# Kernel optimization log

Hardware: AMD Instinct MI355X
Metric: run time of the kernel (lower is better)

## Reference

```python
import jax, jax.numpy as jnp
import numpy as np

N_EMBD = 2048
N_HEAD = 16
HEAD_DIM = N_EMBD // N_HEAD
MAX_SEQ = 2048
ROPE_BASE = 10000.0


def _build_rope_cache(seq_len, head_dim, base):
    theta = 1.0 / (base ** (jnp.arange(0, head_dim, 2, dtype=jnp.float32) / head_dim))
    idx_theta = jnp.arange(seq_len, dtype=jnp.float32)[:, None] * theta[None, :]  # [T, hd/2]
    return jnp.cos(idx_theta), jnp.sin(idx_theta)


def _apply_rope(x, cos, sin):
    # x: [B, T, H, hd]; interleaved (even, odd) pairing along last dim
    B, T, H, hd = x.shape
    xf = x.astype(jnp.float32).reshape(B, T, H, hd // 2, 2)
    x0, x1 = xf[..., 0], xf[..., 1]
    c = cos[None, :T, None, :]
    s = sin[None, :T, None, :]
    out = jnp.stack([x0 * c - x1 * s, x1 * c + x0 * s], axis=-1)
    return out.reshape(B, T, H, hd).astype(x.dtype)


def setup_inputs() -> dict:
    key = jax.random.key(0)
    k1, k2, k3 = jax.random.split(key, 3)
    x = jax.random.normal(k1, (2, 2048, N_EMBD), dtype=jnp.float32)
    # torch Linear(D, 3D, bias=False): y = x @ W.T ; store as [D, 3D] for x @ W
    scale = 1.0 / np.sqrt(N_EMBD)
    w_attn = jax.random.normal(k2, (N_EMBD, 3 * N_EMBD), dtype=jnp.float32) * scale
    w_proj = jax.random.normal(k3, (N_EMBD, N_EMBD), dtype=jnp.float32) * scale
    return {"x": x, "w_attn": w_attn, "w_proj": w_proj}


def reference(x, w_attn, w_proj):
    B, T, D = x.shape
    cos, sin = _build_rope_cache(MAX_SEQ, HEAD_DIM, ROPE_BASE)
    qkv = x @ w_attn                                   # [B, T, 3D]
    q, k, v = jnp.split(qkv, 3, axis=-1)
    q = q.reshape(B, T, N_HEAD, HEAD_DIM)
    k = k.reshape(B, T, N_HEAD, HEAD_DIM)
    v = v.reshape(B, T, N_HEAD, HEAD_DIM)
    q = _apply_rope(q, cos, sin)
    k = _apply_rope(k, cos, sin)
    # non-causal SDPA (original calls F.sdpa without is_causal)
    scale = 1.0 / jnp.sqrt(jnp.asarray(HEAD_DIM, dtype=q.dtype))
    scores = jnp.einsum("bqhd,bkhd->bhqk", q, k) * scale
    attn = jax.nn.softmax(scores, axis=-1)
    y = jnp.einsum("bhqk,bkhd->bqhd", attn, v).reshape(B, T, D)
    return y @ w_proj
```

## Files before the change

### kernel.cpp

```cpp
#include <hip/hip_runtime.h>
#include <cstdint>
#include <cstddef>

typedef __attribute__((ext_vector_type(8))) short bf16x8;
typedef __attribute__((ext_vector_type(8))) unsigned short us8;
typedef __attribute__((ext_vector_type(4))) float f32x4;

#define TSEQ 2048

__device__ __forceinline__ unsigned short f2bf(float f) {
  union { float f; uint32_t u; } v; v.f = f;
  uint32_t u = v.u;
  uint32_t r = (u + 0x7FFFu + ((u >> 16) & 1u)) >> 16;
  return (unsigned short)r;
}
__device__ __forceinline__ unsigned short f2bf_trunc(float f) {
  union { float f; uint32_t u; } v; v.f = f;
  return (unsigned short)(v.u >> 16);
}
__device__ __forceinline__ float bf2f(unsigned short h) {
  union { uint32_t u; float f; } v; v.u = ((uint32_t)h) << 16;
  return v.f;
}

__device__ __forceinline__ void async16(const void* g, void* l) {
  __builtin_amdgcn_global_load_lds(
      (const __attribute__((address_space(1))) unsigned int*)g,
      (__attribute__((address_space(3))) unsigned int*)l,
      16, 0, 0);
}

__global__ __launch_bounds__(256) void cvt_x(
    const float* __restrict__ in, unsigned short* __restrict__ out)
{
  const size_t i = ((size_t)blockIdx.x * 256 + threadIdx.x) * 16;
  f32x4 a0 = *(const f32x4*)(in + i);
  f32x4 a1 = *(const f32x4*)(in + i + 4);
  f32x4 a2 = *(const f32x4*)(in + i + 8);
  f32x4 a3 = *(const f32x4*)(in + i + 12);
  us8 lo, hi;
#pragma unroll
  for (int j = 0; j < 4; j++) {
    lo[j] = f2bf(a0[j]); lo[j + 4] = f2bf(a1[j]);
    hi[j] = f2bf(a2[j]); hi[j + 4] = f2bf(a3[j]);
  }
  *(us8*)(out + i) = lo;
  *(us8*)(out + i + 8) = hi;
}

__global__ __launch_bounds__(256) void transpose_w(
    const float* __restrict__ in, unsigned short* __restrict__ out,
    int R, int C)
{
  __shared__ unsigned short tile[32][33];
  const int bx = blockIdx.x * 32;
  const int by = blockIdx.y * 32;
  const int tx = threadIdx.x & 31;
  const int ty = threadIdx.x >> 5;
#pragma unroll
  for (int r = ty; r < 32; r += 8)
    tile[r][tx] = f2bf(in[(size_t)(by + r) * C + bx + tx]);
  __syncthreads();
#pragma unroll
  for (int r = ty; r < 32; r += 8)
    out[(size_t)(bx + r) * R + by + tx] = tile[tx][r];
}

template <int CF32>
__global__ __launch_bounds__(256) void gemm_bt(
    const unsigned short* __restrict__ A,
    const unsigned short* __restrict__ Bt,
    void* __restrict__ Cv,
    int M, int N, int K, int ldc)
{
  __shared__ unsigned short As[2][128 * 32];
  __shared__ unsigned short Bs[2][128 * 32];
  const int tid  = threadIdx.x;
  const int lane = tid & 63;
  const int w    = tid >> 6;
  const int m0   = blockIdx.y * 128;
  const int n0   = blockIdx.x * 128;
  const int wm   = (w & 1) * 64;
  const int wn   = (w >> 1) * 64;

  const int srow = lane >> 2;
  const int scol = (lane & 3) * 8;
  const unsigned short* ga0 = A  + (size_t)(m0 + w * 16 + srow) * K + scol;
  const unsigned short* ga1 = ga0 + (size_t)64 * K;
  const unsigned short* gb0 = Bt + (size_t)(n0 + w * 16 + srow) * K + scol;
  const unsigned short* gb1 = gb0 + (size_t)64 * K;

  f32x4 acc[4][4];
#pragma unroll
  for (int i = 0; i < 4; i++)
#pragma unroll
    for (int j = 0; j < 4; j++) acc[i][j] = (f32x4){0.f, 0.f, 0.f, 0.f};

  const int frow = lane & 15;
  const int fcol = (lane >> 4) * 8;

  for (int kt = 0; kt < K; kt += 64) {
    __syncthreads();
    async16(ga0 + kt,      &As[0][w * 512]);
    async16(ga1 + kt,      &As[0][(4 + w) * 512]);
    async16(ga0 + kt + 32, &As[1][w * 512]);
    async16(ga1 + kt + 32, &As[1][(4 + w) * 512]);
    async16(gb0 + kt,      &Bs[0][w * 512]);
    async16(gb1 + kt,      &Bs[0][(4 + w) * 512]);
    async16(gb0 + kt + 32, &Bs[1][w * 512]);
    async16(gb1 + kt + 32, &Bs[1][(4 + w) * 512]);
    __syncthreads();

#pragma unroll
    for (int h = 0; h < 2; h++) {
      bf16x8 af[4], bfr[4];
#pragma unroll
      for (int i = 0; i < 4; i++)
        af[i] = *(const bf16x8*)&As[h][(wm + i * 16 + frow) * 32 + fcol];
#pragma unroll
      for (int i = 0; i < 4; i++)
        bfr[i] = *(const bf16x8*)&Bs[h][(wn + i * 16 + frow) * 32 + fcol];
#pragma unroll
      for (int mi = 0; mi < 4; mi++)
#pragma unroll
        for (int ni = 0; ni < 4; ni++)
          acc[mi][ni] = __builtin_amdgcn_mfma_f32_16x16x32_bf16(
              af[mi], bfr[ni], acc[mi][ni], 0, 0, 0);
    }
  }

  const int crow0 = m0 + wm + (lane >> 4) * 4;
  const int ccol0 = n0 + wn + (lane & 15);
  if (CF32) {
    float* Cf = (float*)Cv;
#pragma unroll
    for (int mi = 0; mi < 4; mi++)
#pragma unroll
      for (int i = 0; i < 4; i++) {
        const int row = crow0 + mi * 16 + i;
#pragma unroll
        for (int ni = 0; ni < 4; ni++)
          Cf[(size_t)row * ldc + ccol0 + ni * 16] = acc[mi][ni][i];
      }
  } else {
    unsigned short* Cb = (unsigned short*)Cv;
#pragma unroll
    for (int mi = 0; mi < 4; mi++)
#pragma unroll
      for (int i = 0; i < 4; i++) {
        const int row = crow0 + mi * 16 + i;
#pragma unroll
        for (int ni = 0; ni < 4; ni++)
          Cb[(size_t)row * ldc + ccol0 + ni * 16] = f2bf(acc[mi][ni][i]);
      }
  }
}

__global__ __launch_bounds__(256) void rope_qk(unsigned short* __restrict__ qkv)
{
  const int p   = blockIdx.x * 256 + threadIdx.x;
  const int row = p >> 11;
  const int col = (p & 2047) * 2;
  const int t   = row & (TSEQ - 1);
  const int hd  = col & 127;
  const float theta = powf(10000.0f, -(float)hd * (1.0f / 128.0f));
  const float ang   = (float)t * theta;
  float s, c;
  sincosf(ang, &s, &c);
  const float sc = (col < 2048) ? 0.08838834764831845f : 1.0f;
  uint32_t* ptr = (uint32_t*)(qkv + (size_t)row * 6144 + col);
  const uint32_t u = *ptr;
  const float x0 = bf2f((unsigned short)(u & 0xffffu));
  const float x1 = bf2f((unsigned short)(u >> 16));
  const float o0 = (x0 * c - x1 * s) * sc;
  const float o1 = (x1 * c + x0 * s) * sc;
  *ptr = (uint32_t)f2bf(o0) | ((uint32_t)f2bf(o1) << 16);
}

__global__ __launch_bounds__(256) void repack_v(
    const unsigned short* __restrict__ qkv, unsigned short* __restrict__ Vtg)
{
  __shared__ unsigned short tile[32][33];
  const int tt = blockIdx.x * 32;
  const int dd = blockIdx.y * 32;
  const int bh = blockIdx.z;
  const int b  = bh >> 4, h = bh & 15;
  const int tx = threadIdx.x & 31;
  const int ty = threadIdx.x >> 5;
#pragma unroll
  for (int r = ty; r < 32; r += 8)
    tile[r][tx] = qkv[(size_t)(b * TSEQ + tt + r) * 6144 + 4096 + h * 128 + dd + tx];
  __syncthreads();
#pragma unroll
  for (int r = ty; r < 32; r += 8)
    Vtg[(size_t)bh * 262144 + (size_t)(dd + r) * TSEQ + tt + tx] = tile[tx][r];
}

__global__ __launch_bounds__(256) void attn(
    const unsigned short* __restrict__ qkv,
    const unsigned short* __restrict__ Vtg,
    unsigned short* __restrict__ y)
{
  __shared__ unsigned short Ks[64 * 136];
  __shared__ unsigned short Vs[144 * 72];
  __shared__ unsigned short Ps[4][32 * 72];

  const int tid  = threadIdx.x;
  const int lane = tid & 63;
  const int w    = tid >> 6;
  const int q0   = blockIdx.x * 128;
  const int h    = blockIdx.y;
  const int b    = blockIdx.z;
  const int bh   = b * 16 + h;
  const int quad = lane >> 4;
  const int l15  = lane & 15;
  const int kq   = quad * 8;

  for (int idx = tid; idx < 16 * 72; idx += 256)
    Vs[128 * 72 + idx] = (idx < 72) ? (unsigned short)0x3F80 : (unsigned short)0;

  bf16x8 qa[2][4];
#pragma unroll
  for (int mt = 0; mt < 2; mt++) {
    const unsigned short* gQ =
        qkv + (size_t)(b * TSEQ + q0 + w * 32 + mt * 16 + l15) * 6144 + h * 128 + kq;
#pragma unroll
    for (int dc = 0; dc < 4; dc++) qa[mt][dc] = *(const bf16x8*)(gQ + dc * 32);
  }

  f32x4 ot[2][9];
#pragma unroll
  for (int mt = 0; mt < 2; mt++)
#pragma unroll
    for (int nt = 0; nt < 9; nt++) ot[mt][nt] = (f32x4){0.f, 0.f, 0.f, 0.f};

  const int krow = tid >> 2;
  const int kd   = (tid & 3) * 32;
  const unsigned short* gK = qkv + (size_t)(b * TSEQ) * 6144 + 2048 + h * 128 + kd;
  const int vd = tid >> 1;
  const int vc = (tid & 1) * 32;
  const unsigned short* gVt = Vtg + (size_t)bh * 262144 + (size_t)vd * TSEQ + vc;

  for (int kb = 0; kb < TSEQ; kb += 64) {
    __syncthreads();
    {
      const unsigned short* pk = gK + (size_t)(kb + krow) * 6144;
#pragma unroll
      for (int j = 0; j < 4; j++)
        *(us8*)&Ks[krow * 136 + kd + j * 8] = *(const us8*)(pk + j * 8);
      const unsigned short* pv = gVt + kb;
#pragma unroll
      for (int j = 0; j < 4; j++)
        *(us8*)&Vs[vd * 72 + vc + j * 8] = *(const us8*)(pv + j * 8);
    }
    __syncthreads();

    f32x4 s[2][4];
#pragma unroll
    for (int mt = 0; mt < 2; mt++)
#pragma unroll
      for (int ct = 0; ct < 4; ct++) s[mt][ct] = (f32x4){0.f, 0.f, 0.f, 0.f};
#pragma unroll
    for (int dc = 0; dc < 4; dc++) {
#pragma unroll
      for (int ct = 0; ct < 4; ct++) {
        bf16x8 kf = *(const bf16x8*)&Ks[(ct * 16 + l15) * 136 + dc * 32 + kq];
        s[0][ct] = __builtin_amdgcn_mfma_f32_16x16x32_bf16(qa[0][dc], kf, s[0][ct], 0, 0, 0);
        s[1][ct] = __builtin_amdgcn_mfma_f32_16x16x32_bf16(qa[1][dc], kf, s[1][ct], 0, 0, 0);
      }
    }

    unsigned short* pw = &Ps[w][0];
#pragma unroll
    for (int mt = 0; mt < 2; mt++)
#pragma unroll
      for (int ct = 0; ct < 4; ct++)
#pragma unroll
        for (int i = 0; i < 4; i++)
          pw[(mt * 16 + quad * 4 + i) * 72 + ct * 16 + l15] =
              f2bf_trunc(__expf(fminf(s[mt][ct][i], 30.f)));

    __asm__ volatile("s_waitcnt lgkmcnt(0)" ::: "memory");

#pragma unroll
    for (int kc = 0; kc < 2; kc++) {
      bf16x8 pa0 = *(const bf16x8*)&pw[(l15) * 72 + kc * 32 + kq];
      bf16x8 pa1 = *(const bf16x8*)&pw[(16 + l15) * 72 + kc * 32 + kq];
#pragma unroll
      for (int nt = 0; nt < 9; nt++) {
        bf16x8 vb = *(const bf16x8*)&Vs[(nt * 16 + l15) * 72 + kc * 32 + kq];
        ot[0][nt] = __builtin_amdgcn_mfma_f32_16x16x32_bf16(pa0, vb, ot[0][nt], 0, 0, 0);
        ot[1][nt] = __builtin_amdgcn_mfma_f32_16x16x32_bf16(pa1, vb, ot[1][nt], 0, 0, 0);
      }
    }
  }

#pragma unroll
  for (int mt = 0; mt < 2; mt++) {
    unsigned short* gy =
        y + (size_t)(b * TSEQ + q0 + w * 32 + mt * 16 + quad * 4) * 2048 + h * 128 + l15;
#pragma unroll
    for (int i = 0; i < 4; i++) {
      const float inv = 1.0f / __shfl(ot[mt][8][i], lane & 48);
#pragma unroll
      for (int nt = 0; nt < 8; nt++)
        gy[(size_t)i * 2048 + nt * 16] = f2bf(ot[mt][nt][i] * inv);
    }
  }
}

extern "C" void kernel_launch(void* const* d_in, const int* in_sizes, int n_in,
                              void* d_out, int out_size, void* d_ws, size_t ws_size,
                              hipStream_t stream)
{
  const float* x      = (const float*)d_in[0];
  const float* w_attn = (const float*)d_in[1];
  const float* w_proj = (const float*)d_in[2];

  if (ws_size < 67108864u) return;

  char* ws = (char*)d_ws;
  unsigned short* qkv = (unsigned short*)(ws);
  unsigned short* xb  = (unsigned short*)(ws + 50331648);
  unsigned short* y   = xb;
  unsigned short* wT2 = (unsigned short*)(ws);
  unsigned short* wTa = (unsigned short*)d_out;
  unsigned short* Vtg = (unsigned short*)d_out;

  transpose_w<<<dim3(192, 64), 256, 0, stream>>>(w_attn, wTa, 2048, 6144);
  cvt_x<<<dim3(2048), 256, 0, stream>>>(x, xb);
  gemm_bt<0><<<dim3(48, 32), 256, 0, stream>>>(xb, wTa, (void*)qkv, 4096, 6144, 2048, 6144);
  rope_qk<<<dim3(32768), 256, 0, stream>>>(qkv);
  repack_v<<<dim3(64, 4, 32), 256, 0, stream>>>(qkv, Vtg);
  attn<<<dim3(16, 16, 2), 256, 0, stream>>>(qkv, Vtg, y);
  transpose_w<<<dim3(64, 64), 256, 0, stream>>>(w_proj, wT2, 2048, 2048);
  gemm_bt<1><<<dim3(16, 32), 256, 0, stream>>>(y, wT2, d_out, 4096, 2048, 2048, 2048);
}
```

Baseline: 450.8 us.

## Replace QKV GEMM with 256x256-tile double-buffered async MFMA kernel

Adds a new 512-thread GEMM that computes 256x256 output tiles. It uses double-buffered async global-to-LDS staging, XOR-swizzled LDS reads, an XCD-aware workgroup remap and priority-raised MFMA phases. The QKV projection now uses it instead of the 128-tile gemm_bt, aiming for more data reuse per load and better overlap of loads with compute. RoPE's powf is also replaced with exp2f, which costs fewer instructions but may differ slightly in rounding. The larger tiles use much more LDS and registers, which limits occupancy, and only 384 workgroups are launched.

```diff
diff --git a/kernel.cpp b/kernel.cpp
--- a/kernel.cpp
+++ b/kernel.cpp
@@ -156,6 +156,156 @@
   }
 }
 
+__device__ __forceinline__ void stage8(
+    const unsigned short* gA, const unsigned short* gB,
+    unsigned short* asb, unsigned short* bsb, int K, int kt, int lw)
+{
+#pragma unroll
+  for (int j = 0; j < 4; j++)
+    async16(gA + (size_t)j * 64 * K + (size_t)kt * 64, asb + j * 4096 + lw);
+#pragma unroll
+  for (int j = 0; j < 4; j++)
+    async16(gB + (size_t)j * 64 * K + (size_t)kt * 64, bsb + j * 4096 + lw);
+}
+
+__global__ __launch_bounds__(512, 2) void gemm256(
+    const unsigned short* __restrict__ A,
+    const unsigned short* __restrict__ Bt,
+    unsigned short* __restrict__ C,
+    int K, int ldc, int ntiles, int nwg)
+{
+  __shared__ unsigned short As[2][256 * 64];
+  __shared__ unsigned short Bs[2][256 * 64];
+
+  int wg = blockIdx.x;
+  wg = (wg & 7) * (nwg >> 3) + (wg >> 3);
+  const int m0 = (wg / ntiles) * 256;
+  const int n0 = (wg % ntiles) * 256;
+
+  const int tid  = threadIdx.x;
+  const int lane = tid & 63;
+  const int w    = tid >> 6;
+  const int wr   = w & 1;
+  const int wc   = w >> 1;
+
+  const int srow  = tid >> 3;
+  const int sslot = (tid ^ srow) & 7;
+  const unsigned short* gA = A  + (size_t)(m0 + srow) * K + sslot * 8;
+  const unsigned short* gB = Bt + (size_t)(n0 + srow) * K + sslot * 8;
+  const int lw = w * 512;
+
+  f32x4 acc[8][4];
+#pragma unroll
+  for (int i = 0; i < 8; i++)
+#pragma unroll
+    for (int j = 0; j < 4; j++) acc[i][j] = (f32x4){0.f, 0.f, 0.f, 0.f};
+
+  const int frow = lane & 15;
+  const int fq16 = (lane >> 4) * 16;
+  const int axr  = (frow & 7) << 4;
+  const int arow = (wr * 128 + frow) * 128;
+  const int brow = (wc * 64 + frow) * 128;
+
+#define RDA(buf, mi, kh) \
+  (*(const bf16x8*)((const char*)&As[buf][0] + ((arow + (mi) * 2048 + (kh) * 64 + fq16) ^ axr)))
+#define RDB(buf, ni, kh) \
+  (*(const bf16x8*)((const char*)&Bs[buf][0] + ((brow + (ni) * 2048 + (kh) * 64 + fq16) ^ axr)))
+
+  stage8(gA, gB, &As[0][0], &Bs[0][0], K, 0, lw);
+  stage8(gA, gB, &As[1][0], &Bs[1][0], K, 1, lw);
+  asm volatile("s_waitcnt vmcnt(8)" ::: "memory");
+  __builtin_amdgcn_s_barrier();
+
+  const int NT = K >> 6;
+  bf16x8 a[4][2], b[4][2];
+  for (int kt = 0; kt < NT; ++kt) {
+    const int p = kt & 1;
+
+#pragma unroll
+    for (int mi = 0; mi < 4; mi++) { a[mi][0] = RDA(p, mi, 0); a[mi][1] = RDA(p, mi, 1); }
+#pragma unroll
+    for (int ni = 0; ni < 2; ni++) { b[ni][0] = RDB(p, ni, 0); b[ni][1] = RDB(p, ni, 1); }
+    __builtin_amdgcn_s_barrier();
+    asm volatile("s_waitcnt lgkmcnt(0)" ::: "memory");
+    __builtin_amdgcn_s_setprio(1);
+#pragma unroll
+    for (int mi = 0; mi < 4; mi++)
+#pragma unroll
+      for (int ni = 0; ni < 2; ni++)
+#pragma unroll
+        for (int kh = 0; kh < 2; kh++)
+          acc[mi][ni] = __builtin_amdgcn_mfma_f32_16x16x32_bf16(
+              a[mi][kh], b[ni][kh], acc[mi][ni], 0, 0, 0);
+    __builtin_amdgcn_s_setprio(0);
+    __builtin_amdgcn_s_barrier();
+
+#pragma unroll
+    for (int ni = 2; ni < 4; ni++) { b[ni][0] = RDB(p, ni, 0); b[ni][1] = RDB(p, ni, 1); }
+    __builtin_amdgcn_s_barrier();
+    asm volatile("s_waitcnt lgkmcnt(0)" ::: "memory");
+    __builtin_amdgcn_s_setprio(1);
+#pragma unroll
+    for (int mi = 0; mi < 4; mi++)
+#pragma unroll
+      for (int ni = 2; ni < 4; ni++)
+#pragma unroll
+        for (int kh = 0; kh < 2; kh++)
+          acc[mi][ni] = __builtin_amdgcn_mfma_f32_16x16x32_bf16(
+              a[mi][kh], b[ni][kh], acc[mi][ni], 0, 0, 0);
+    __builtin_amdgcn_s_setprio(0);
+    __builtin_amdgcn_s_barrier();
+
+#pragma unroll
+    for (int mi = 0; mi < 4; mi++) { a[mi][0] = RDA(p, mi + 4, 0); a[mi][1] = RDA(p, mi + 4, 1); }
+    __builtin_amdgcn_s_barrier();
+    asm volatile("s_waitcnt lgkmcnt(0)" ::: "memory");
+    __builtin_amdgcn_s_setprio(1);
+#pragma unroll
+    for (int mi = 0; mi < 4; mi++)
+#pragma unroll
+      for (int ni = 2; ni < 4; ni++)
+#pragma unroll
+        for (int kh = 0; kh < 2; kh++)
+          acc[mi + 4][ni] = __builtin_amdgcn_mfma_f32_16x16x32_bf16(
+              a[mi][kh], b[ni][kh], acc[mi + 4][ni], 0, 0, 0);
+    __builtin_amdgcn_s_setprio(0);
+    __builtin_amdgcn_s_barrier();
+
+    if (kt + 2 < NT)
+      stage8(gA, gB, &As[p][0], &Bs[p][0], K, kt + 2, lw);
+    __builtin_amdgcn_s_setprio(1);
+#pragma unroll
+    for (int mi = 0; mi < 4; mi++)
+#pragma unroll
+      for (int ni = 0; ni < 2; ni++)
+#pragma unroll
+        for (int kh = 0; kh < 2; kh++)
+          acc[mi + 4][ni] = __builtin_amdgcn_mfma_f32_16x16x32_bf16(
+              a[mi][kh], b[ni][kh], acc[mi + 4][ni], 0, 0, 0);
+    __builtin_amdgcn_s_setprio(0);
+    if (kt + 2 < NT) {
+      asm volatile("s_waitcnt vmcnt(8)" ::: "memory");
+    } else {
+      asm volatile("s_waitcnt vmcnt(0)" ::: "memory");
+    }
+    __builtin_amdgcn_s_barrier();
+  }
+#undef RDA
+#undef RDB
+
+  const int crow0 = m0 + wr * 128 + (lane >> 4) * 4;
+  const int ccol0 = n0 + wc * 64 + frow;
+#pragma unroll
+  for (int mi = 0; mi < 8; mi++)
+#pragma unroll
+    for (int i = 0; i < 4; i++) {
+      const size_t row = (size_t)(crow0 + mi * 16 + i);
+#pragma unroll
+      for (int ni = 0; ni < 4; ni++)
+        C[row * ldc + ccol0 + ni * 16] = f2bf(acc[mi][ni][i]);
+    }
+}
+
 __global__ __launch_bounds__(256) void rope_qk(unsigned short* __restrict__ qkv)
 {
   const int p   = blockIdx.x * 256 + threadIdx.x;
@@ -163,7 +313,7 @@
   const int col = (p & 2047) * 2;
   const int t   = row & (TSEQ - 1);
   const int hd  = col & 127;
-  const float theta = powf(10000.0f, -(float)hd * (1.0f / 128.0f));
+  const float theta = exp2f((float)hd * -0.1038102531f);
   const float ang   = (float)t * theta;
   float s, c;
   sincosf(ang, &s, &c);
@@ -329,7 +479,7 @@
 
   transpose_w<<<dim3(192, 64), 256, 0, stream>>>(w_attn, wTa, 2048, 6144);
   cvt_x<<<dim3(2048), 256, 0, stream>>>(x, xb);
-  gemm_bt<0><<<dim3(48, 32), 256, 0, stream>>>(xb, wTa, (void*)qkv, 4096, 6144, 2048, 6144);
+  gemm256<<<dim3(384), 512, 0, stream>>>(xb, wTa, qkv, 2048, 6144, 24, 384);
   rope_qk<<<dim3(32768), 256, 0, stream>>>(qkv);
   repack_v<<<dim3(64, 4, 32), 256, 0, stream>>>(qkv, Vtg);
   attn<<<dim3(16, 16, 2), 256, 0, stream>>>(qkv, Vtg, y);
```

After: 452.7 us. About the same (+0.4%).
